# Kernel optimization log

Measured on AMD Instinct MI355X. Metric: run time of the kernel, lower is better.

## Reference

```python
import jax, jax.numpy as jnp
import numpy as np
from jax.scipy.special import logsumexp

EPS = 0.05        # entropic regularization (blur^p)
N_ITERS = 20      # Sinkhorn iterations
N, M, D = 8192, 8192, 64


def setup_inputs() -> dict:
    key = jax.random.key(0)
    k1, k2, k3, k4 = jax.random.split(key, 4)
    return {
        "a": jax.random.uniform(k1, (N,), dtype=jnp.float32),
        "x": jax.random.normal(k2, (N, D), dtype=jnp.float32),
        "b": jax.random.uniform(k3, (M,), dtype=jnp.float32),
        "y": jax.random.normal(k4, (M, D), dtype=jnp.float32),
    }


def reference(a, x, b, y):
    eps = EPS
    # _normalize_weights: probability simplex
    a = a / jnp.sum(a)
    b = b / jnp.sum(b)
    loga = jnp.log(a)
    logb = jnp.log(b)
    # squared-Euclidean cost C_ij = ||x_i - y_j||^2, built via one GEMM (online kernel's math)
    x2 = jnp.sum(x * x, axis=1)            # [N]
    y2 = jnp.sum(y * y, axis=1)            # [M]
    C = x2[:, None] + y2[None, :] - 2.0 * (x @ y.T)   # [N, M]

    # log-domain Sinkhorn: f_i = -eps * LSE_j( log b_j + (g_j - C_ij)/eps )
    def softmin_rows(g_, C_, logw):   # reduce over columns j -> [N]
        return -eps * logsumexp(logw[None, :] + (g_[None, :] - C_) / eps, axis=1)

    def softmin_cols(f_, C_, logw):   # reduce over rows i -> [M]
        return -eps * logsumexp(logw[:, None] + (f_[:, None] - C_) / eps, axis=0)

    def body(i, fg):
        f_, g_ = fg
        f_ = softmin_rows(g_, C, logb)
        g_ = softmin_cols(f_, C, loga)
        return (f_, g_)

    f0 = jnp.zeros_like(a)
    g0 = jnp.zeros_like(b)
    f, g = jax.lax.fori_loop(0, N_ITERS, body, (f0, g0))

    # GeomLoss-style: one final symmetric update from detached potentials (Danskin)
    f_d = jax.lax.stop_gradient(f)
    g_d = jax.lax.stop_gradient(g)
    f_fin = softmin_rows(g_d, C, logb)
    g_fin = softmin_cols(f_d, C, loga)
    # OT_eps(a, b) = <a, f> + <b, g>
    return jnp.sum(a * f_fin) + jnp.sum(b * g_fin)
```

## Files before the change

kernel.cpp:

```cpp
#include <hip/hip_runtime.h>
#include <hip/hip_bf16.h>

#define EPS       0.05f
#define N_ITERS   20
#define NR        8192
#define DIM       64
#define LOG2E     1.4426950408889634f
#define LN2       0.6931471805599453f
#define S2        (2.0f * LOG2E / EPS)
#define EPSLN2    (EPS * LN2)
#define NEGINF    (-1e30f)
#define NSPLIT    16

typedef __attribute__((ext_vector_type(8))) short short8;
typedef __attribute__((ext_vector_type(4))) float float4v;

#define GLD_LDS16(src, dst)                                              \
    __builtin_amdgcn_global_load_lds(                                    \
        (const __attribute__((address_space(1))) void*)(src),            \
        (__attribute__((address_space(3))) void*)(dst), 16, 0, 0)

__device__ __forceinline__ float wave_reduce_sum(float v) {
    #pragma unroll
    for (int m = 1; m < 64; m <<= 1) v += __shfl_xor(v, m, 64);
    return v;
}

__device__ __forceinline__ float merge16_l(const float2* __restrict__ P, int i) {
    float2 p[NSPLIT];
    float M = NEGINF;
    #pragma unroll
    for (int k = 0; k < NSPLIT; k++) {
        p[k] = P[k * NR + i];
        M = fmaxf(M, p[k].x);
    }
    float S = 0.f;
    #pragma unroll
    for (int k = 0; k < NSPLIT; k++)
        S += p[k].y * __builtin_amdgcn_exp2f(p[k].x - M);
    return M + __builtin_amdgcn_logf(S);
}

__global__ void sums_kernel(const float* __restrict__ a, const float* __restrict__ b,
                            float* __restrict__ sums) {
    __shared__ float red[32];
    int tid = threadIdx.x;
    float pa = 0.f, pb = 0.f;
    for (int i = tid; i < NR; i += blockDim.x) { pa += a[i]; pb += b[i]; }
    pa = wave_reduce_sum(pa);
    pb = wave_reduce_sum(pb);
    int wid = tid >> 6, ln = tid & 63;
    if (ln == 0) { red[wid] = pa; red[wid + 16] = pb; }
    __syncthreads();
    if (tid == 0) {
        float sa = 0.f, sb = 0.f;
        int nw = blockDim.x >> 6;
        for (int w = 0; w < nw; w++) { sa += red[w]; sb += red[w + 16]; }
        sums[0] = logf(sa); sums[1] = logf(sb); sums[2] = sa; sums[3] = sb;
    }
}

__global__ void prep_kernel(const float* __restrict__ x, const float* __restrict__ y,
                            const float* __restrict__ a, const float* __restrict__ b,
                            const float* __restrict__ sums,
                            short8* __restrict__ xs, short8* __restrict__ ys,
                            float* __restrict__ x2, float* __restrict__ y2,
                            float* __restrict__ la2, float* __restrict__ lb2,
                            float2* __restrict__ Pb) {
    int gid = blockIdx.x * 256 + threadIdx.x;
    bool isx = gid < NR * 8;
    int cid = isx ? gid : gid - NR * 8;
    int row = cid >> 3;
    int c   = cid & 7;
    const float4* src = (const float4*)(isx ? x : y);
    float4 v0 = src[row * 16 + c * 2];
    float4 v1 = src[row * 16 + c * 2 + 1];

    short8 st;
    st[0] = __bfloat16_as_short(__float2bfloat16(v0.x));
    st[1] = __bfloat16_as_short(__float2bfloat16(v0.y));
    st[2] = __bfloat16_as_short(__float2bfloat16(v0.z));
    st[3] = __bfloat16_as_short(__float2bfloat16(v0.w));
    st[4] = __bfloat16_as_short(__float2bfloat16(v1.x));
    st[5] = __bfloat16_as_short(__float2bfloat16(v1.y));
    st[6] = __bfloat16_as_short(__float2bfloat16(v1.z));
    st[7] = __bfloat16_as_short(__float2bfloat16(v1.w));

    int T = row >> 4, ln = row & 15, f = c >> 2, q = c & 3;
    (isx ? xs : ys)[T * 128 + f * 64 + q * 16 + ln] = st;

    float sq = v0.x*v0.x + v0.y*v0.y + v0.z*v0.z + v0.w*v0.w
             + v1.x*v1.x + v1.y*v1.y + v1.z*v1.z + v1.w*v1.w;
    #pragma unroll
    for (int m = 1; m < 8; m <<= 1) sq += __shfl_xor(sq, m, 64);

    if (c == 0) {
        if (isx) {
            x2[row] = sq;
            la2[row] = (logf(a[row]) - sums[0]) * LOG2E;
        } else {
            y2[row] = sq;
            lb2[row] = (logf(b[row]) - sums[1]) * LOG2E;
            Pb[row] = make_float2(sq * (LOG2E / EPS), 1.0f);
            #pragma unroll
            for (int k = 1; k < NSPLIT; k++)
                Pb[k * NR + row] = make_float2(NEGINF, 0.0f);
        }
    }
}

#define LSE4(acc, c4, mm, ss)                                            \
    {                                                                    \
        float z0 = fmaf(S2, (acc)[0], (c4).x);                           \
        float z1 = fmaf(S2, (acc)[1], (c4).y);                           \
        float z2 = fmaf(S2, (acc)[2], (c4).z);                           \
        float z3 = fmaf(S2, (acc)[3], (c4).w);                           \
        float zm = fmaxf(fmaxf(z0, z1), fmaxf(z2, z3));                  \
        float mn = fmaxf((mm), zm);                                      \
        float e  = __builtin_amdgcn_exp2f((mm) - mn);                    \
        float p  = (__builtin_amdgcn_exp2f(z0 - mn)                      \
                  + __builtin_amdgcn_exp2f(z1 - mn))                     \
                 + (__builtin_amdgcn_exp2f(z2 - mn)                      \
                  + __builtin_amdgcn_exp2f(z3 - mn));                    \
        (ss) = fmaf((ss), e, p);                                         \
        (mm) = mn;                                                       \
    }

__global__ __launch_bounds__(1024, 4) void pass_kernel(
        const short8* __restrict__ matXs,
        const short8* __restrict__ matYs,
        const float2* __restrict__ Pin,
        const float* __restrict__ lw2col,
        float2* __restrict__ Pout) {
    __shared__ __attribute__((aligned(16))) char xlds[65536];
    __shared__ __attribute__((aligned(16))) char ybuf[3][16384];
    __shared__ __attribute__((aligned(16))) float cbl[512];
    __shared__ __attribute__((aligned(16))) float2 pm[1024];

    const int tid = threadIdx.x;
    const int bi  = blockIdx.x;
    const int q   = bi & 15;
    const int rg  = bi >> 4;
    const int rb  = rg * 512;
    const int cb0 = q * 512;

    const int w    = tid >> 6;
    const int lane = tid & 63;
    const int quad = lane >> 4;
    const int ln   = lane & 15;
    const int cst  = w & 3;
    const int rq   = w >> 2;

    const int jcol = cb0 + (tid & 511);
    const int hh   = tid >> 9;
    float2 pp[8];
    #pragma unroll
    for (int k = 0; k < 8; k++)
        pp[k] = Pin[(hh * 8 + k) * NR + jcol];
    float lwv = lw2col[jcol];
    __builtin_amdgcn_sched_barrier(0);

    const char* xsrc = (const char*)matXs + (size_t)rb * 128;
    const char* ysrc = (const char*)matYs + (size_t)cb0 * 128;
    #pragma unroll
    for (int r = 0; r < 4; r++)
        GLD_LDS16(xsrc + r * 16384 + tid * 16, &xlds[r * 16384 + w * 1024]);
    GLD_LDS16(ysrc + 0 * 16384 + tid * 16, &ybuf[0][w * 1024]);
    GLD_LDS16(ysrc + 1 * 16384 + tid * 16, &ybuf[1][w * 1024]);
    GLD_LDS16(ysrc + 2 * 16384 + tid * 16, &ybuf[2][w * 1024]);
    __builtin_amdgcn_sched_barrier(0);

    __builtin_amdgcn_s_waitcnt(0x0077);
    __builtin_amdgcn_sched_barrier(0);

    {
        float M = pp[0].x;
        #pragma unroll
        for (int k = 1; k < 8; k++) M = fmaxf(M, pp[k].x);
        float S = 0.f;
        #pragma unroll
        for (int k = 0; k < 8; k++)
            S += pp[k].y * __builtin_amdgcn_exp2f(pp[k].x - M);
        pm[tid] = make_float2(M, S);
    }
    __builtin_amdgcn_sched_barrier(0);
    __builtin_amdgcn_s_waitcnt(0xC07F);
    __builtin_amdgcn_s_barrier();
    __builtin_amdgcn_sched_barrier(0);

    if (tid < 512) {
        float2 h0 = pm[tid];
        float2 h1 = pm[tid + 512];
        float M = fmaxf(h0.x, h1.x);
        float S = h0.y * __builtin_amdgcn_exp2f(h0.x - M)
                + h1.y * __builtin_amdgcn_exp2f(h1.x - M);
        cbl[tid] = lwv - (M + __builtin_amdgcn_logf(S));
    }
    __builtin_amdgcn_sched_barrier(0);
    __builtin_amdgcn_s_waitcnt(0x0072);
    __builtin_amdgcn_s_barrier();
    __builtin_amdgcn_sched_barrier(0);

    short8 xf0[8], xf1[8];
    {
        const char* xw = &xlds[(rq * 8) * 2048];
        #pragma unroll
        for (int t = 0; t < 8; t++) {
            xf0[t] = *(const short8*)(xw + t * 2048 + lane * 16);
            xf1[t] = *(const short8*)(xw + t * 2048 + 1024 + lane * 16);
        }
    }

    float lm[8], ls[8];
    #pragma unroll
    for (int t = 0; t < 8; t++) { lm[t] = NEGINF; ls[t] = 0.f; }

    #pragma unroll
    for (int c = 0; c < 4; c++) {
        const char* base = &ybuf[c % 3][0];
        #pragma unroll
        for (int uu = 0; uu < 2; uu++) {
            const int u = cst * 2 + uu;
            short8 ya0 = *(const short8*)(base + u * 2048 + lane * 16);
            short8 ya1 = *(const short8*)(base + u * 2048 + 1024 + lane * 16);
            float4 c4  = *(const float4*)(cbl + (c * 8 + u) * 16 + quad * 4);

            #pragma unroll
            for (int tt = 0; tt < 8; tt++) {
                float4v acc = {0.f, 0.f, 0.f, 0.f};
                acc = __builtin_amdgcn_mfma_f32_16x16x32_bf16(ya0, xf0[tt], acc, 0, 0, 0);
                acc = __builtin_amdgcn_mfma_f32_16x16x32_bf16(ya1, xf1[tt], acc, 0, 0, 0);
                LSE4(acc, c4, lm[tt], ls[tt]);
            }
        }
        if (c < 3) {
            __builtin_amdgcn_sched_barrier(0);
            __builtin_amdgcn_s_barrier();
            __builtin_amdgcn_sched_barrier(0);
            if (c == 0)
                GLD_LDS16(ysrc + 3 * 16384 + tid * 16, &ybuf[0][w * 1024]);
            __builtin_amdgcn_sched_barrier(0);
            if (c == 0)      __builtin_amdgcn_s_waitcnt(0x0072);
            else if (c == 1) __builtin_amdgcn_s_waitcnt(0x0071);
            else             __builtin_amdgcn_s_waitcnt(0x0070);
            __builtin_amdgcn_s_barrier();
            __builtin_amdgcn_sched_barrier(0);
        }
    }

    #pragma unroll
    for (int mask = 16; mask < 64; mask <<= 1) {
        #pragma unroll
        for (int t = 0; t < 8; t++) {
            float mo = __shfl_xor(lm[t], mask, 64);
            float so = __shfl_xor(ls[t], mask, 64);
            float M  = fmaxf(lm[t], mo);
            ls[t] = ls[t] * __builtin_amdgcn_exp2f(lm[t] - M)
                  + so    * __builtin_amdgcn_exp2f(mo    - M);
            lm[t] = M;
        }
    }

    float2 (*comb)[5] = (float2(*)[5])xlds;
    __syncthreads();
    if (lane < 16) {
        #pragma unroll
        for (int t = 0; t < 8; t++)
            comb[rq * 128 + t * 16 + ln][cst] = make_float2(lm[t], ls[t]);
    }
    __syncthreads();

    if (tid < 512) {
        float2 cc0 = comb[tid][0];
        float M = cc0.x, S = cc0.y;
        #pragma unroll
        for (int cc = 1; cc < 4; cc++) {
            float2 p = comb[tid][cc];
            float Mn = fmaxf(M, p.x);
            S = S * __builtin_amdgcn_exp2f(M - Mn)
              + p.y * __builtin_amdgcn_exp2f(p.x - Mn);
            M = Mn;
        }
        Pout[q * NR + rb + tid] = make_float2(M, S);
    }
}

__global__ void reduce1_kernel(const float* __restrict__ a, const float* __restrict__ b,
                               const float* __restrict__ x2, const float* __restrict__ y2,
                               const float2* __restrict__ Pff, const float2* __restrict__ Pgf,
                               float2* __restrict__ red2) {
    __shared__ float red[4];
    int tid = threadIdx.x;
    int r   = blockIdx.x * 128 + (tid & 127);
    bool gs = tid >= 128;
    float L  = merge16_l(gs ? Pgf : Pff, r);
    float sq = gs ? y2[r] : x2[r];
    float wv = gs ? b[r]  : a[r];
    float v  = wv * (sq - EPSLN2 * L);
    v = wave_reduce_sum(v);
    if ((tid & 63) == 0) red[tid >> 6] = v;
    __syncthreads();
    if (tid == 0) red2[blockIdx.x] = make_float2(red[0] + red[1], red[2] + red[3]);
}

__global__ void reduce2_kernel(const float* __restrict__ sums,
                               const float2* __restrict__ red2,
                               float* __restrict__ out) {
    int tid = threadIdx.x;
    float2 v = red2[tid];
    float da = wave_reduce_sum(v.x);
    float db = wave_reduce_sum(v.y);
    if (tid == 0) out[0] = da / sums[2] + db / sums[3];
}

extern "C" void kernel_launch(void* const* d_in, const int* in_sizes, int n_in,
                              void* d_out, int out_size, void* d_ws, size_t ws_size,
                              hipStream_t stream) {
    const float* a = (const float*)d_in[0];
    const float* x = (const float*)d_in[1];
    const float* b = (const float*)d_in[2];
    const float* y = (const float*)d_in[3];

    char* ws = (char*)d_ws;
    short8* xs = (short8*)ws;
    short8* ys = (short8*)(ws + (1 << 20));
    float* fp  = (float*)(ws + (2 << 20));
    float* x2  = fp;
    float* y2  = fp + NR;
    float* la2 = fp + 2 * NR;
    float* lb2 = fp + 3 * NR;
    float2* P   = (float2*)(fp + 4 * NR);
    float2* Pf  = P;
    float2* Pb  = P + NSPLIT * NR;
    float2* Pff = P + 2 * NSPLIT * NR;
    float2* Pgf = P + 3 * NSPLIT * NR;
    float2* red2 = P + 4 * NSPLIT * NR;
    float* sums  = (float*)(red2 + 64);

    sums_kernel<<<1, 1024, 0, stream>>>(a, b, sums);
    prep_kernel<<<(2 * NR * 8) / 256, 256, 0, stream>>>(x, y, a, b, sums,
                                                        xs, ys,
                                                        x2, y2, la2, lb2, Pb);

    for (int it = 0; it < N_ITERS; it++) {
        pass_kernel<<<256, 1024, 0, stream>>>(xs, ys, Pb, lb2, Pf);
        pass_kernel<<<256, 1024, 0, stream>>>(ys, xs, Pf, la2, Pb);
    }
    pass_kernel<<<256, 1024, 0, stream>>>(xs, ys, Pb, lb2, Pff);
    pass_kernel<<<256, 1024, 0, stream>>>(ys, xs, Pf, la2, Pgf);

    reduce1_kernel<<<64, 256, 0, stream>>>(a, b, x2, y2, Pff, Pgf, red2);
    reduce2_kernel<<<1, 64, 0, stream>>>(sums, red2, (float*)d_out);
}
```

Measured before the change: 875.6 us.

## Replace direct global-to-LDS loads with register-staged loads and explicit LDS stores

Swaps the global_load_lds async copies for ordinary vector global loads into registers, followed by explicit ds_write stores into the x and y LDS buffers. The y tile pipeline is restructured so the next chunk is prefetched into a register while the current chunk is computed, with writes and barriers moved to the start of each chunk iteration. This is meant to avoid the costs or limits of the direct-to-LDS path and give finer control over overlap. It adds register pressure, extra LDS write instructions and an extra barrier per chunk, and the hand-written waitcnt values must match the new load counts exactly.

```diff
diff --git a/kernel.cpp b/kernel.cpp
--- a/kernel.cpp
+++ b/kernel.cpp
@@ -14,11 +14,6 @@
 
 typedef __attribute__((ext_vector_type(8))) short short8;
 typedef __attribute__((ext_vector_type(4))) float float4v;
-
-#define GLD_LDS16(src, dst)                                              \
-    __builtin_amdgcn_global_load_lds(                                    \
-        (const __attribute__((address_space(1))) void*)(src),            \
-        (__attribute__((address_space(3))) void*)(dst), 16, 0, 0)
 
 __device__ __forceinline__ float wave_reduce_sum(float v) {
     #pragma unroll
@@ -162,15 +157,16 @@
 
     const char* xsrc = (const char*)matXs + (size_t)rb * 128;
     const char* ysrc = (const char*)matYs + (size_t)cb0 * 128;
+    short8 xst[4];
     #pragma unroll
     for (int r = 0; r < 4; r++)
-        GLD_LDS16(xsrc + r * 16384 + tid * 16, &xlds[r * 16384 + w * 1024]);
-    GLD_LDS16(ysrc + 0 * 16384 + tid * 16, &ybuf[0][w * 1024]);
-    GLD_LDS16(ysrc + 1 * 16384 + tid * 16, &ybuf[1][w * 1024]);
-    GLD_LDS16(ysrc + 2 * 16384 + tid * 16, &ybuf[2][w * 1024]);
-    __builtin_amdgcn_sched_barrier(0);
-
-    __builtin_amdgcn_s_waitcnt(0x0077);
+        xst[r] = *(const short8*)(xsrc + r * 16384 + tid * 16);
+    __builtin_amdgcn_sched_barrier(0);
+    short8 yst0 = *(const short8*)(ysrc + 0 * 16384 + tid * 16);
+    short8 ynext = *(const short8*)(ysrc + 1 * 16384 + tid * 16);
+    __builtin_amdgcn_sched_barrier(0);
+
+    __builtin_amdgcn_s_waitcnt(0x0076);
     __builtin_amdgcn_sched_barrier(0);
 
     {
@@ -197,7 +193,16 @@
         cbl[tid] = lwv - (M + __builtin_amdgcn_logf(S));
     }
     __builtin_amdgcn_sched_barrier(0);
+
     __builtin_amdgcn_s_waitcnt(0x0072);
+    #pragma unroll
+    for (int r = 0; r < 4; r++)
+        *(short8*)(&xlds[r * 16384 + tid * 16]) = xst[r];
+    __builtin_amdgcn_sched_barrier(0);
+    __builtin_amdgcn_s_waitcnt(0x0071);
+    *(short8*)(&ybuf[0][tid * 16]) = yst0;
+    __builtin_amdgcn_sched_barrier(0);
+    __builtin_amdgcn_s_waitcnt(0xC07F);
     __builtin_amdgcn_s_barrier();
     __builtin_amdgcn_sched_barrier(0);
 
@@ -217,6 +222,23 @@
 
     #pragma unroll
     for (int c = 0; c < 4; c++) {
+        if (c > 0) {
+            __builtin_amdgcn_sched_barrier(0);
+            __builtin_amdgcn_s_barrier();
+            __builtin_amdgcn_sched_barrier(0);
+        }
+        if (c < 3) {
+            __builtin_amdgcn_s_waitcnt(0x0070);
+            *(short8*)(&ybuf[(c + 1) % 3][tid * 16]) = ynext;
+            __builtin_amdgcn_sched_barrier(0);
+            if (c < 2)
+                ynext = *(const short8*)(ysrc + (c + 2) * 16384 + tid * 16);
+            __builtin_amdgcn_sched_barrier(0);
+            __builtin_amdgcn_s_waitcnt(0xC07F);
+            __builtin_amdgcn_s_barrier();
+            __builtin_amdgcn_sched_barrier(0);
+        }
+
         const char* base = &ybuf[c % 3][0];
         #pragma unroll
         for (int uu = 0; uu < 2; uu++) {
@@ -232,19 +254,6 @@
                 acc = __builtin_amdgcn_mfma_f32_16x16x32_bf16(ya1, xf1[tt], acc, 0, 0, 0);
                 LSE4(acc, c4, lm[tt], ls[tt]);
             }
-        }
-        if (c < 3) {
-            __builtin_amdgcn_sched_barrier(0);
-            __builtin_amdgcn_s_barrier();
-            __builtin_amdgcn_sched_barrier(0);
-            if (c == 0)
-                GLD_LDS16(ysrc + 3 * 16384 + tid * 16, &ybuf[0][w * 1024]);
-            __builtin_amdgcn_sched_barrier(0);
-            if (c == 0)      __builtin_amdgcn_s_waitcnt(0x0072);
-            else if (c == 1) __builtin_amdgcn_s_waitcnt(0x0071);
-            else             __builtin_amdgcn_s_waitcnt(0x0070);
-            __builtin_amdgcn_s_barrier();
-            __builtin_amdgcn_sched_barrier(0);
         }
     }
 
```

New measurement: 910.1 us. +3.9%, slower.
